# Optimization experiments

Hardware: AMD Instinct MI355X
Metric: run time of the kernel (lower is better)

## Reference

```python
import jax, jax.numpy as jnp
import numpy as np

D, H = 2048, 16
Q_RANK, KV_RANK = 1536, 512
NOPE, ROPE_D, V_D = 128, 64, 128
QK_D = NOPE + ROPE_D  # 192
S, B = 2048, 1
THETA = 10000.0
EPS = 1e-5


def rmsnorm(x, w, eps=EPS):
    return x * jax.lax.rsqrt(jnp.mean(x * x, -1, keepdims=True) + eps) * w


def rope_cos_sin(s, d, theta=THETA):
    inv = 1.0 / (theta ** (jnp.arange(0, d, 2, dtype=jnp.float32) / d))
    f = jnp.arange(s, dtype=jnp.float32)[:, None] * inv[None, :]  # [s, d//2]
    emb = jnp.concatenate([f, f], -1)  # [s, d]
    return jnp.cos(emb), jnp.sin(emb)


def apply_rope(x, cos, sin):
    # DeepSeek-V3 variant: de-interleave consecutive pairs into [even | odd] halves first
    b, h, s, d = x.shape
    x = x.reshape(b, h, s, d // 2, 2).transpose(0, 1, 2, 4, 3).reshape(b, h, s, d)
    x1, x2 = jnp.split(x, 2, -1)
    rot = jnp.concatenate([-x2, x1], -1)
    return x * cos + rot * sin


def setup_inputs() -> dict:
    key = jax.random.key(0)
    ks = jax.random.split(key, 10)
    s = 0.02
    return {
        "x": jax.random.normal(ks[0], (S, B, D), jnp.float32),
        "norm1_w": jnp.ones((D,), jnp.float32),
        "q_a_w": jax.random.normal(ks[1], (D, Q_RANK), jnp.float32) * s,
        "q_a_ln_w": jnp.ones((Q_RANK,), jnp.float32),
        "q_b_w": jax.random.normal(ks[2], (Q_RANK, H * QK_D), jnp.float32) * s,
        "kv_a_w": jax.random.normal(ks[3], (D, KV_RANK + ROPE_D), jnp.float32) * s,
        "kv_a_ln_w": jnp.ones((KV_RANK,), jnp.float32),
        "kv_b_w": jax.random.normal(ks[4], (KV_RANK, H * (NOPE + V_D)), jnp.float32) * s,
        "o_w": jax.random.normal(ks[5], (H * V_D, D), jnp.float32) * s,
        "norm2_w": jnp.ones((D,), jnp.float32),
        "ffn_w1": jax.random.normal(ks[6], (D, 4 * D), jnp.float32) * s,
        "ffn_b1": jnp.zeros((4 * D,), jnp.float32),
        "ffn_w2": jax.random.normal(ks[7], (4 * D, D), jnp.float32) * s,
        "ffn_b2": jnp.zeros((D,), jnp.float32),
    }


def reference(x, norm1_w, q_a_w, q_a_ln_w, q_b_w, kv_a_w, kv_a_ln_w, kv_b_w, o_w,
              norm2_w, ffn_w1, ffn_b1, ffn_w2, ffn_b2):
    # x: [S, B, D] (block transposes to [B, S, D] before MLA)
    hs = jnp.swapaxes(rmsnorm(x, norm1_w), 0, 1)  # [B, S, D]
    b, s, _ = hs.shape

    # --- MLA: low-rank Q and KV with decoupled RoPE ---
    q = rmsnorm(hs @ q_a_w, q_a_ln_w) @ q_b_w                    # [B, S, H*192]
    q = q.reshape(b, s, H, QK_D).transpose(0, 2, 1, 3)           # [B, H, S, 192]
    q_nope, q_pe = q[..., :NOPE], q[..., NOPE:]

    kv_a = hs @ kv_a_w                                           # [B, S, 576]
    c_kv, k_pe = kv_a[..., :KV_RANK], kv_a[..., KV_RANK:]        # [B,S,512], [B,S,64]
    kv = rmsnorm(c_kv, kv_a_ln_w) @ kv_b_w                       # [B, S, H*256]
    kv = kv.reshape(b, s, H, NOPE + V_D).transpose(0, 2, 1, 3)   # [B, H, S, 256]
    k_nope, v = kv[..., :NOPE], kv[..., NOPE:]

    cos, sin = rope_cos_sin(s, ROPE_D)
    q_pe = apply_rope(q_pe, cos, sin)                            # [B, H, S, 64]
    k_pe = apply_rope(k_pe[:, None, :, :], cos, sin)             # [B, 1, S, 64]

    q_full = jnp.concatenate([q_nope, q_pe], -1)                 # [B, H, S, 192]
    k_full = jnp.concatenate([k_nope, jnp.broadcast_to(k_pe, (b, H, s, ROPE_D))], -1)

    scores = jnp.einsum('bhqd,bhkd->bhqk', q_full, k_full) * (1.0 / np.sqrt(QK_D))
    causal = jnp.tril(jnp.ones((s, s), bool))
    scores = jnp.where(causal, scores, jnp.finfo(scores.dtype).min)
    attn = jax.nn.softmax(scores, -1)
    out = jnp.einsum('bhqk,bhkd->bhqd', attn, v)                 # [B, H, S, 128]
    out = out.transpose(0, 2, 1, 3).reshape(b, s, H * V_D) @ o_w # [B, S, D]

    x = x + jnp.swapaxes(out, 0, 1)                              # residual, back to [S,B,D]

    # --- FFN (exact GELU) ---
    h2 = rmsnorm(x, norm2_w)
    ffn = jax.nn.gelu(h2 @ ffn_w1 + ffn_b1, approximate=False) @ ffn_w2 + ffn_b2
    return x + ffn
```

## Files before the change

kernel.cpp:

```cpp
#include <hip/hip_runtime.h>
#include <hip/hip_bf16.h>

typedef __hip_bfloat16 bf16;
using bf16x8 = __attribute__((ext_vector_type(8))) __bf16;
using f32x4  = __attribute__((ext_vector_type(4))) float;

#define S_   2048
#define D_   2048
#define H_   16
#define QR_  1536
#define KVR_ 512
#define NOPE_ 128
#define ROPE_ 64
#define VD_  128
#define QKD_ 192
#define EPS_ 1e-5f
#define QKVN 2112

#define GLDS16(g, l) \
    __builtin_amdgcn_global_load_lds((const __attribute__((address_space(1))) void*)(g), \
                                     (__attribute__((address_space(3))) void*)(l), 16, 0, 0)

#define PIPE_WAIT4 asm volatile("s_waitcnt vmcnt(4)\n\ts_barrier" ::: "memory")
#define PIPE_WAIT0 asm volatile("s_waitcnt vmcnt(0)\n\ts_barrier" ::: "memory")

__global__ __launch_bounds__(256) void gemm_k(
    const bf16* __restrict__ A, const bf16* __restrict__ BT, void* __restrict__ Cv,
    const float* __restrict__ bias, const float* __restrict__ res,
    int M, int N, int K, int lda, int ldb, int ldc,
    long long strideA, long long strideB, long long strideC,
    int mode, int causal, int ksplit, int kchunk)
{
    int bn = blockIdx.x, bm = blockIdx.y;
    int bzC = blockIdx.z;
    int bz = bzC, kc = 0;
    if (ksplit > 1) { kc = bzC % ksplit; bz = bzC / ksplit; }
    if (causal == 1 && bn > bm) return;
    A  += (size_t)bz * strideA;
    BT += (size_t)bz * strideB;

    int k_end = K;
    if (causal == 2) { int kl = (bm + 1) * 128; if (kl < k_end) k_end = kl; }
    int k_begin = kc * kchunk;
    if (k_begin + kchunk < k_end) k_end = k_begin + kchunk;
    if (k_begin >= k_end) return;
    int nIter = (k_end - k_begin) >> 5;

    __shared__ bf16 sA[3 * 128 * 32];
    __shared__ bf16 sB[3 * 128 * 32];

    int tid  = threadIdx.x;
    int lane = tid & 63, wave = tid >> 6;
    int wr = wave >> 1, wc = wave & 1;
    int fr = lane & 15, fq = lane >> 4;

    int row0 = bm * 128, col0 = bn * 128;

    int srow = wave * 16 + (lane >> 2);
    int sko  = (lane & 3) * 8;
    const bf16* ga0 = A + (size_t)(row0 + srow) * lda + sko;
    const bf16* ga1 = ga0 + (size_t)64 * lda;
    int bn0 = col0 + srow;      if (bn0 > N - 1) bn0 = N - 1;
    int bn1 = col0 + srow + 64; if (bn1 > N - 1) bn1 = N - 1;
    const bf16* gb0 = BT + (size_t)bn0 * ldb + sko;
    const bf16* gb1 = BT + (size_t)bn1 * ldb + sko;
    bf16* lA0 = &sA[(wave * 16) * 32];
    bf16* lA1 = &sA[(64 + wave * 16) * 32];
    bf16* lB0 = &sB[(wave * 16) * 32];
    bf16* lB1 = &sB[(64 + wave * 16) * 32];

#define STAGE(ofs, k0) do {                  \
        GLDS16(ga0 + (k0), lA0 + (ofs));     \
        GLDS16(ga1 + (k0), lA1 + (ofs));     \
        GLDS16(gb0 + (k0), lB0 + (ofs));     \
        GLDS16(gb1 + (k0), lB1 + (ofs));     \
    } while (0)

    f32x4 acc[4][4] = {};

#define COMPUTE(ofs) do {                                                           \
        bf16x8 af[4], bv[4];                                                        \
        _Pragma("unroll")                                                           \
        for (int i = 0; i < 4; ++i)                                                 \
            af[i] = *(const bf16x8*)&sA[(ofs) + (wr*64 + i*16 + fr)*32 + fq*8];     \
        _Pragma("unroll")                                                           \
        for (int j = 0; j < 4; ++j)                                                 \
            bv[j] = *(const bf16x8*)&sB[(ofs) + (wc*64 + j*16 + fr)*32 + fq*8];     \
        _Pragma("unroll")                                                           \
        for (int i = 0; i < 4; ++i)                                                 \
            _Pragma("unroll")                                                       \
            for (int j = 0; j < 4; ++j)                                             \
                acc[i][j] = __builtin_amdgcn_mfma_f32_16x16x32_bf16(af[i], bv[j], acc[i][j], 0, 0, 0); \
    } while (0)

    STAGE(0, k_begin);
    if (nIter > 1) STAGE(4096, k_begin + 32);

    int curo = 0, pfo = 8192;
    int it = 0;
    for (; it < nIter - 1; ++it) {
        PIPE_WAIT4;
        if (it + 2 < nIter) STAGE(pfo, k_begin + (it + 2) * 32);
        COMPUTE(curo);
        curo += 4096; if (curo == 12288) curo = 0;
        pfo  += 4096; if (pfo  == 12288) pfo  = 0;
    }
    PIPE_WAIT0;
    COMPUTE(curo);
#undef STAGE
#undef COMPUTE

    #pragma unroll
    for (int i = 0; i < 4; ++i) {
        #pragma unroll
        for (int j = 0; j < 4; ++j) {
            int gc = col0 + wc*64 + j*16 + fr;
            if (gc >= N) continue;
            #pragma unroll
            for (int r = 0; r < 4; ++r) {
                int gr = row0 + wr*64 + i*16 + fq*4 + r;
                float v = acc[i][j][r];
                size_t off = (size_t)bzC * strideC + (size_t)gr * ldc + gc;
                if (mode == 0 || mode == 6) {
                    ((float*)Cv)[off] = v;
                } else if (mode == 1) {
                    ((bf16*)Cv)[off] = __float2bfloat16(v);
                } else if (mode == 2) {
                    ((float*)Cv)[off] = v + res[(size_t)gr * ldc + gc];
                } else if (mode == 3) {
                    float t = v + bias[gc];
                    t = 0.5f * t * (1.0f + erff(t * 0.70710678118654752f));
                    ((bf16*)Cv)[off] = __float2bfloat16(t);
                } else {
                    ((float*)Cv)[off] = v + bias[gc] + res[(size_t)gr * ldc + gc];
                }
            }
        }
    }
}

__global__ __launch_bounds__(512, 2) void gemm256_k(
    const bf16* __restrict__ A, const bf16* __restrict__ BT, void* __restrict__ Cv,
    const float* __restrict__ bias,
    int M, int N, int K, int lda, int ldb, int ldc,
    long long strideC, int mode, int kchunk)
{
    int bn = blockIdx.x, bm = blockIdx.y, kc = blockIdx.z;
    int k_begin = kc * kchunk;
    int k_end = (k_begin + kchunk < K) ? (k_begin + kchunk) : K;
    int NT = (k_end - k_begin) >> 6;

    __shared__ __align__(16) bf16 sA[2 * 256 * 64];
    __shared__ __align__(16) bf16 sB[2 * 256 * 64];

    int tid = threadIdx.x;
    int lane = tid & 63, w = tid >> 6;
    int wr = w >> 2, wc = w & 3;
    int fr = lane & 15, fq = lane >> 4;
    int row0 = bm * 256, col0 = bn * 256;

    int g0 = tid, g1 = tid + 512;
    int r0 = g0 >> 3, l0 = (g0 & 7) ^ (r0 & 7);
    int r1 = g1 >> 3, l1 = (g1 & 7) ^ (r1 & 7);
    const bf16* gA00 = A + (size_t)(row0 + r0) * lda + k_begin + l0 * 8;
    const bf16* gA01 = A + (size_t)(row0 + r1) * lda + k_begin + l1 * 8;
    const bf16* gA10 = gA00 + (size_t)128 * lda;
    const bf16* gA11 = gA01 + (size_t)128 * lda;
    int c00 = col0 + r0;       if (c00 > N - 1) c00 = N - 1;
    int c01 = col0 + r1;       if (c01 > N - 1) c01 = N - 1;
    int c10 = col0 + 128 + r0; if (c10 > N - 1) c10 = N - 1;
    int c11 = col0 + 128 + r1; if (c11 > N - 1) c11 = N - 1;
    const bf16* gB00 = BT + (size_t)c00 * ldb + k_begin + l0 * 8;
    const bf16* gB01 = BT + (size_t)c01 * ldb + k_begin + l1 * 8;
    const bf16* gB10 = BT + (size_t)c10 * ldb + k_begin + l0 * 8;
    const bf16* gB11 = BT + (size_t)c11 * ldb + k_begin + l1 * 8;

#define ST_HALF(arr, bofs, p0, p1, t) do {                                  \
        GLDS16((p0) + (size_t)(t) * 64, (arr) + (bofs) + w * 512);          \
        GLDS16((p1) + (size_t)(t) * 64, (arr) + (bofs) + w * 512 + 4096);   \
    } while (0)
#define ST_A0(b, t) ST_HALF(sA, (b) * 16384,        gA00, gA01, t)
#define ST_A1(b, t) ST_HALF(sA, (b) * 16384 + 8192, gA10, gA11, t)
#define ST_B0(b, t) ST_HALF(sB, (b) * 16384,        gB00, gB01, t)
#define ST_B1(b, t) ST_HALF(sB, (b) * 16384 + 8192, gB10, gB11, t)

    int arow = (wr * 128 + fr) * 64;
    int brow = (wc * 64 + fr) * 64;
    int pk0 = (fq ^ (fr & 7)) * 8;
    int pk1 = pk0 ^ 32;

    f32x4 acc[8][4] = {};

#define MFMA_Q(AF, BF, IOFF, JOFF) do {                                     \
        __builtin_amdgcn_s_setprio(1);                                      \
        _Pragma("unroll")                                                   \
        for (int m = 0; m < 4; ++m)                                         \
            _Pragma("unroll")                                               \
            for (int n = 0; n < 2; ++n)                                     \
                acc[(IOFF)+m][(JOFF)+n] = __builtin_amdgcn_mfma_f32_16x16x32_bf16( \
                    AF[m][0], BF[n][0], acc[(IOFF)+m][(JOFF)+n], 0, 0, 0);  \
        _Pragma("unroll")                                                   \
        for (int m = 0; m < 4; ++m)                                         \
            _Pragma("unroll")                                               \
            for (int n = 0; n < 2; ++n)                                     \
                acc[(IOFF)+m][(JOFF)+n] = __builtin_amdgcn_mfma_f32_16x16x32_bf16( \
                    AF[m][1], BF[n][1], acc[(IOFF)+m][(JOFF)+n], 0, 0, 0);  \
        __builtin_amdgcn_s_setprio(0);                                      \
    } while (0)

    ST_A0(0, 0); ST_A1(0, 0); ST_B0(0, 0); ST_B1(0, 0);
    if (NT > 1) { ST_B0(1, 1); ST_B1(1, 1); ST_A0(1, 1); }
    if (NT > 1) asm volatile("s_waitcnt vmcnt(6)" ::: "memory");
    else        asm volatile("s_waitcnt vmcnt(0)" ::: "memory");
    __builtin_amdgcn_s_barrier();

    for (int t = 0; t < NT; ++t) {
        int buf = t & 1;
        int sbase = buf * 16384;
        bf16x8 af[4][2], blo[2][2], bhi[2][2];

        #pragma unroll
        for (int m = 0; m < 4; ++m) {
            af[m][0] = *(const bf16x8*)&sA[sbase + arow + m*1024 + pk0];
            af[m][1] = *(const bf16x8*)&sA[sbase + arow + m*1024 + pk1];
        }
        #pragma unroll
        for (int n = 0; n < 2; ++n) {
            blo[n][0] = *(const bf16x8*)&sB[sbase + brow + n*1024 + pk0];
            blo[n][1] = *(const bf16x8*)&sB[sbase + brow + n*1024 + pk1];
        }
        if (t + 1 < NT) ST_A1((t + 1) & 1, t + 1);
        asm volatile("s_waitcnt lgkmcnt(8)" ::: "memory");
        __builtin_amdgcn_s_barrier();
        asm volatile("s_waitcnt lgkmcnt(0)" ::: "memory");
        __builtin_amdgcn_sched_barrier(0);
        MFMA_Q(af, blo, 0, 0);
        __builtin_amdgcn_s_barrier();

        #pragma unroll
        for (int n = 0; n < 2; ++n) {
            bhi[n][0] = *(const bf16x8*)&sB[sbase + brow + (n+2)*1024 + pk0];
            bhi[n][1] = *(const bf16x8*)&sB[sbase + brow + (n+2)*1024 + pk1];
        }
        if (t + 2 < NT) ST_B0(buf, t + 2);
        __builtin_amdgcn_s_barrier();
        asm volatile("s_waitcnt lgkmcnt(0)" ::: "memory");
        __builtin_amdgcn_sched_barrier(0);
        MFMA_Q(af, bhi, 0, 2);
        __builtin_amdgcn_s_barrier();

        #pragma unroll
        for (int m = 0; m < 4; ++m) {
            af[m][0] = *(const bf16x8*)&sA[sbase + arow + 4096 + m*1024 + pk0];
            af[m][1] = *(const bf16x8*)&sA[sbase + arow + 4096 + m*1024 + pk1];
        }
        if (t + 2 < NT) ST_B1(buf, t + 2);
        __builtin_amdgcn_s_barrier();
        asm volatile("s_waitcnt lgkmcnt(0)" ::: "memory");
        __builtin_amdgcn_sched_barrier(0);
        MFMA_Q(af, blo, 4, 0);
        __builtin_amdgcn_s_barrier();

        if (t + 2 < NT) ST_A0(buf, t + 2);
        if (t < NT - 2) asm volatile("s_waitcnt vmcnt(6)" ::: "memory");
        else            asm volatile("s_waitcnt vmcnt(0)" ::: "memory");
        __builtin_amdgcn_s_barrier();
        MFMA_Q(af, bhi, 4, 2);
        __builtin_amdgcn_s_barrier();
    }
#undef MFMA_Q
#undef ST_A0
#undef ST_A1
#undef ST_B0
#undef ST_B1
#undef ST_HALF

    #pragma unroll
    for (int i = 0; i < 8; ++i) {
        #pragma unroll
        for (int j = 0; j < 4; ++j) {
            int gc = col0 + wc*64 + j*16 + fr;
            if (gc >= N) continue;
            #pragma unroll
            for (int r = 0; r < 4; ++r) {
                int gr = row0 + wr*128 + i*16 + fq*4 + r;
                float v = acc[i][j][r];
                size_t off = (size_t)kc * strideC + (size_t)gr * ldc + gc;
                if (mode == 0 || mode == 6) {
                    ((float*)Cv)[off] = v;
                } else if (mode == 1) {
                    ((bf16*)Cv)[off] = __float2bfloat16(v);
                } else {
                    float tt = v + bias[gc];
                    tt = 0.5f * tt * (1.0f + erff(tt * 0.70710678118654752f));
                    ((bf16*)Cv)[off] = __float2bfloat16(tt);
                }
            }
        }
    }
}

__global__ __launch_bounds__(256) void red_k(const float* __restrict__ part,
        long long pstride4, int nch, const float* __restrict__ res,
        const float* __restrict__ bias, long long cols4,
        float* __restrict__ dstF, bf16* __restrict__ dstB, long long n4)
{
    long long i = (long long)blockIdx.x * 256 + threadIdx.x;
    long long stride = (long long)gridDim.x * 256;
    for (; i < n4; i += stride) {
        float4 v = ((const float4*)part)[i];
        for (int k = 1; k < nch; ++k) {
            float4 p = ((const float4*)part)[i + k * pstride4];
            v.x += p.x; v.y += p.y; v.z += p.z; v.w += p.w;
        }
        if (res) {
            float4 rr = ((const float4*)res)[i];
            v.x += rr.x; v.y += rr.y; v.z += rr.z; v.w += rr.w;
        }
        if (bias) {
            float4 b = ((const float4*)bias)[i % cols4];
            v.x += b.x; v.y += b.y; v.z += b.z; v.w += b.w;
        }
        if (dstB) {
            ushort4 o;
            bf16 t0 = __float2bfloat16(v.x); o.x = *(unsigned short*)&t0;
            bf16 t1 = __float2bfloat16(v.y); o.y = *(unsigned short*)&t1;
            bf16 t2 = __float2bfloat16(v.z); o.z = *(unsigned short*)&t2;
            bf16 t3 = __float2bfloat16(v.w); o.w = *(unsigned short*)&t3;
            ((ushort4*)dstB)[i] = o;
        } else {
            ((float4*)dstF)[i] = v;
        }
    }
}

__global__ __launch_bounds__(128) void pv_red(const float* __restrict__ part,
                                              bf16* __restrict__ ao, int grp)
{
    int r = blockIdx.x, head = blockIdx.y, d = threadIdx.x;
    int nv = ((r >> 7) + 4) >> 2;
    const float* p = part + ((size_t)head * 4) * S_ * VD_ + (size_t)r * VD_ + d;
    float s = 0.f;
    for (int k = 0; k < nv; ++k) s += p[(size_t)k * S_ * VD_];
    ao[(size_t)r * (H_ * VD_) + grp * 1024 + head * VD_ + d] = __float2bfloat16(s);
}

__global__ __launch_bounds__(256) void transpose_w(const float* __restrict__ in,
                                                   bf16* __restrict__ out, int R, int C)
{
    __shared__ float t[32][33];
    int c0 = blockIdx.x * 32, r0 = blockIdx.y * 32;
    int tx = threadIdx.x, ty = threadIdx.y;
    for (int j = ty; j < 32; j += 8) {
        int r = r0 + j, c = c0 + tx;
        t[j][tx] = (r < R && c < C) ? in[(size_t)r * C + c] : 0.f;
    }
    __syncthreads();
    for (int j = ty; j < 32; j += 8) {
        int c = c0 + j, r = r0 + tx;
        if (c < C && r < R) out[(size_t)c * R + r] = __float2bfloat16(t[tx][j]);
    }
}

__global__ __launch_bounds__(256) void transpose_v(const bf16* __restrict__ kv,
                                                   bf16* __restrict__ vT)
{
    __shared__ bf16 t[32][33];
    int h = blockIdx.z;
    int d0 = blockIdx.x * 32, s0 = blockIdx.y * 32;
    int tx = threadIdx.x, ty = threadIdx.y;
    for (int j = ty; j < 32; j += 8)
        t[j][tx] = kv[(size_t)(s0 + j) * (H_*256) + h*256 + 128 + d0 + tx];
    __syncthreads();
    for (int j = ty; j < 32; j += 8)
        vT[((size_t)h * VD_ + d0 + j) * S_ + s0 + tx] = t[tx][j];
}

__global__ __launch_bounds__(256) void rmsnorm_k(const float* __restrict__ in,
                                                 const float* __restrict__ w,
                                                 bf16* __restrict__ out,
                                                 int cols, int istride, int ostride)
{
    int row = blockIdx.x, tid = threadIdx.x;
    const float* ip = in + (size_t)row * istride;
    bf16* op = out + (size_t)row * ostride;
    float ss = 0.f;
    for (int c = tid; c < cols; c += 256) { float v = ip[c]; ss = fmaf(v, v, ss); }
    for (int o = 32; o > 0; o >>= 1) ss += __shfl_down(ss, o, 64);
    __shared__ float red[4];
    __shared__ float s_sc;
    int wave = tid >> 6, lane = tid & 63;
    if (lane == 0) red[wave] = ss;
    __syncthreads();
    if (tid == 0) s_sc = rsqrtf((red[0]+red[1]+red[2]+red[3]) / (float)cols + EPS_);
    __syncthreads();
    float sc = s_sc;
    for (int c = tid; c < cols; c += 256)
        op[c] = __float2bfloat16(ip[c] * sc * w[c]);
}

#define ROPE_LC 0.28782313662425575f

__global__ __launch_bounds__(192) void build_q(const bf16* __restrict__ q,
                                               bf16* __restrict__ qf)
{
    int s = blockIdx.x, h = blockIdx.y, t = threadIdx.x;
    const float scale = 0.07216878364870323f;
    const bf16* src = q + (size_t)s * (H_*QKD_) + h * QKD_;
    bf16* dst = qf + ((size_t)h * S_ + s) * QKD_;
    if (t < NOPE_) {
        dst[t] = __float2bfloat16(__bfloat162float(src[t]) * scale);
    } else {
        int i = (t - NOPE_) & 31;
        bool hi = (t - NOPE_) >= 32;
        float a = __bfloat162float(src[NOPE_ + 2*i]);
        float b = __bfloat162float(src[NOPE_ + 2*i + 1]);
        float inv = __expf(-(float)i * ROPE_LC);
        float f = (float)s * inv, c, sn;
        sincosf(f, &sn, &c);
        float v = hi ? (b * c + a * sn) : (a * c - b * sn);
        dst[t] = __float2bfloat16(v * scale);
    }
}

__global__ __launch_bounds__(192) void build_k(const bf16* __restrict__ kv,
                                               const float* __restrict__ qakva32,
                                               bf16* __restrict__ kf)
{
    int s = blockIdx.x, h = blockIdx.y, t = threadIdx.x;
    const bf16* src = kv + (size_t)s * (H_*256) + h * 256;
    bf16* dst = kf + ((size_t)h * S_ + s) * QKD_;
    if (t < NOPE_) {
        dst[t] = src[t];
    } else {
        int i = (t - NOPE_) & 31;
        bool hi = (t - NOPE_) >= 32;
        const float* pe = qakva32 + (size_t)s * QKVN + (QR_ + KVR_);
        float a = pe[2*i], b = pe[2*i + 1];
        float inv = __expf(-(float)i * ROPE_LC);
        float f = (float)s * inv, c, sn;
        sincosf(f, &sn, &c);
        dst[t] = __float2bfloat16(hi ? (b * c + a * sn) : (a * c - b * sn));
    }
}

__global__ __launch_bounds__(256) void softmax_k(bf16* __restrict__ Sc)
{
    int q = blockIdx.x, h = blockIdx.y;
    bf16* row = Sc + ((size_t)h * S_ + q) * S_;
    int n = q + 1;
    int klim = ((q >> 7) + 1) << 7;
    int tid = threadIdx.x, lane = tid & 63, wave = tid >> 6;
    __shared__ float red[4];
    __shared__ float bc;

    float v[8];
    #pragma unroll
    for (int k = 0; k < 8; ++k) {
        int c = tid + k * 256;
        v[k] = (c < n) ? __bfloat162float(row[c]) : -3.0e38f;
    }
    float mx = v[0];
    #pragma unroll
    for (int k = 1; k < 8; ++k) mx = fmaxf(mx, v[k]);
    for (int o = 32; o > 0; o >>= 1) mx = fmaxf(mx, __shfl_down(mx, o, 64));
    if (lane == 0) red[wave] = mx;
    __syncthreads();
    if (tid == 0) bc = fmaxf(fmaxf(red[0], red[1]), fmaxf(red[2], red[3]));
    __syncthreads();
    float m = bc;
    float sum = 0.f;
    #pragma unroll
    for (int k = 0; k < 8; ++k) {
        int c = tid + k * 256;
        v[k] = (c < n) ? __expf(v[k] - m) : 0.f;
        sum += v[k];
    }
    for (int o = 32; o > 0; o >>= 1) sum += __shfl_down(sum, o, 64);
    __syncthreads();
    if (lane == 0) red[wave] = sum;
    __syncthreads();
    if (tid == 0) bc = 1.0f / (red[0] + red[1] + red[2] + red[3]);
    __syncthreads();
    float inv = bc;
    #pragma unroll
    for (int k = 0; k < 8; ++k) {
        int c = tid + k * 256;
        if (c < klim) row[c] = __float2bfloat16(c < n ? v[k] * inv : 0.f);
    }
}

static inline void gemm(hipStream_t st, const bf16* A, const bf16* BT, void* C,
                        const float* bias, const float* res,
                        int M, int N, int K, int lda, int ldb, int ldc,
                        long long sA, long long sB, long long sC,
                        int batch, int mode, int causal, int ksplit = 1, int kchunk = 0)
{
    if (kchunk == 0) kchunk = K;
    dim3 g((N + 127) / 128, M / 128, batch * ksplit);
    gemm_k<<<g, 256, 0, st>>>(A, BT, C, bias, res, M, N, K, lda, ldb, ldc,
                              sA, sB, sC, mode, causal, ksplit, kchunk);
}

static inline void gemm256(hipStream_t st, const bf16* A, const bf16* BT, void* C,
                           const float* bias, int M, int N, int K,
                           int lda, int ldb, int ldc, long long sC,
                           int mode, int ksplit = 1, int kchunk = 0)
{
    if (kchunk == 0) kchunk = K;
    dim3 g((N + 255) / 256, M / 256, ksplit);
    gemm256_k<<<g, 512, 0, st>>>(A, BT, C, bias, M, N, K, lda, ldb, ldc,
                                 sC, mode, kchunk);
}

static inline void transw(hipStream_t st, const float* in, bf16* out, int R, int C)
{
    dim3 g((C + 31) / 32, (R + 31) / 32);
    transpose_w<<<g, dim3(32, 8), 0, st>>>(in, out, R, C);
}

extern "C" void kernel_launch(void* const* d_in, const int* in_sizes, int n_in,
                              void* d_out, int out_size, void* d_ws, size_t ws_size,
                              hipStream_t stream)
{
    const float* x        = (const float*)d_in[0];
    const float* norm1_w  = (const float*)d_in[1];
    const float* q_a_w    = (const float*)d_in[2];
    const float* q_a_ln_w = (const float*)d_in[3];
    const float* q_b_w    = (const float*)d_in[4];
    const float* kv_a_w   = (const float*)d_in[5];
    const float* kv_a_ln_w= (const float*)d_in[6];
    const float* kv_b_w   = (const float*)d_in[7];
    const float* o_w      = (const float*)d_in[8];
    const float* norm2_w  = (const float*)d_in[9];
    const float* ffn_w1   = (const float*)d_in[10];
    const float* ffn_b1   = (const float*)d_in[11];
    const float* ffn_w2   = (const float*)d_in[12];
    const float* ffn_b2   = (const float*)d_in[13];
    float* out = (float*)d_out;

    size_t off = 0;
    auto alloc = [&](size_t bytes) -> void* {
        void* p = (char*)d_ws + off;
        off += (bytes + 255) & ~(size_t)255;
        return p;
    };
    bf16*  hs     = (bf16*) alloc((size_t)S_*D_*2);
    bf16*  wqakvT = (bf16*) alloc((size_t)QKVN*D_*2);
    bf16*  wqbT   = (bf16*) alloc((size_t)(H_*QKD_)*QR_*2);
    bf16*  wkvbT  = (bf16*) alloc((size_t)(H_*(NOPE_+VD_))*KVR_*2);
    bf16*  woT    = (bf16*) alloc((size_t)D_*(H_*VD_)*2);
    bf16*  wf1T   = (bf16*) alloc((size_t)(4*D_)*D_*2);
    bf16*  wf2T   = (bf16*) alloc((size_t)D_*(4*D_)*2);
    float* qakva32= (float*)alloc((size_t)S_*QKVN*4);
    bf16*  qln    = (bf16*) alloc((size_t)S_*QR_*2);
    bf16*  kvln   = (bf16*) alloc((size_t)S_*KVR_*2);
    bf16*  qb     = (bf16*) alloc((size_t)S_*H_*QKD_*2);
    bf16*  kvb    = (bf16*) alloc((size_t)S_*H_*(NOPE_+VD_)*2);
    bf16*  qf     = (bf16*) alloc((size_t)H_*S_*QKD_*2);
    bf16*  kf     = (bf16*) alloc((size_t)H_*S_*QKD_*2);
    bf16*  vT     = (bf16*) alloc((size_t)H_*VD_*S_*2);
    bf16*  Sc     = (bf16*) alloc((size_t)8*S_*S_*2);
    float* qakvaP = (float*)Sc;
    float* qbP    = (float*)Sc;
    float* pvP    = (float*)qakva32;
    float* oP     = (float*)Sc;
    float* f2P    = (float*)d_ws;
    float* x2     = qakva32;
    bf16*  h2     = qb;
    bf16*  ao     = kvb;
    bf16*  a1     = Sc;

    transw(stream, q_a_w,  wqakvT,                    D_,  QR_);
    transw(stream, kv_a_w, wqakvT + (size_t)QR_ * D_, D_,  KVR_+ROPE_);
    transw(stream, q_b_w,  wqbT,  QR_, H_*QKD_);
    transw(stream, kv_b_w, wkvbT, KVR_, H_*(NOPE_+VD_));
    transw(stream, o_w,    woT,   H_*VD_, D_);
    transw(stream, ffn_w1, wf1T,  D_,  4*D_);
    transw(stream, ffn_w2, wf2T,  4*D_, D_);

    rmsnorm_k<<<S_, 256, 0, stream>>>(x, norm1_w, hs, D_, D_, D_);

    gemm256(stream, hs, wqakvT, qakvaP, nullptr, S_, QKVN, D_, D_, D_, QKVN,
            (long long)S_*QKVN, 6, 3, 768);
    red_k<<<1024, 256, 0, stream>>>(qakvaP, (long long)S_*QKVN/4, 3, nullptr, nullptr, 1,
                                    qakva32, nullptr, (long long)S_*QKVN/4);

    rmsnorm_k<<<S_, 256, 0, stream>>>(qakva32, q_a_ln_w, qln, QR_, QKVN, QR_);
    gemm256(stream, qln, wqbT, qbP, nullptr, S_, H_*QKD_, QR_, QR_, QR_, H_*QKD_,
            (long long)S_*(H_*QKD_), 6, 2, 768);
    red_k<<<1024, 256, 0, stream>>>(qbP, (long long)S_*(H_*QKD_)/4, 2, nullptr, nullptr, 1,
                                    nullptr, qb, (long long)S_*(H_*QKD_)/4);

    rmsnorm_k<<<S_, 256, 0, stream>>>(qakva32 + QR_, kv_a_ln_w, kvln, KVR_, QKVN, KVR_);
    gemm(stream, kvln, wkvbT, kvb, nullptr, nullptr, S_, H_*(NOPE_+VD_), KVR_,
         KVR_, KVR_, H_*(NOPE_+VD_), 0, 0, 0, 1, 1, 0);

    build_q<<<dim3(S_, H_), 192, 0, stream>>>(qb, qf);
    build_k<<<dim3(S_, H_), 192, 0, stream>>>(kvb, qakva32, kf);
    transpose_v<<<dim3(VD_/32, S_/32, H_), dim3(32, 8), 0, stream>>>(kvb, vT);

    for (int g = 0; g < 2; ++g) {
        const bf16* qfg = qf + (size_t)g * 8 * S_ * QKD_;
        const bf16* kfg = kf + (size_t)g * 8 * S_ * QKD_;
        const bf16* vTg = vT + (size_t)g * 8 * VD_ * S_;
        gemm(stream, qfg, kfg, Sc, nullptr, nullptr,
             S_, S_, QKD_, QKD_, QKD_, S_,
             (long long)S_*QKD_, (long long)S_*QKD_, (long long)S_*S_, 8, 1, 1);
        softmax_k<<<dim3(S_, 8), 256, 0, stream>>>(Sc);
        gemm(stream, Sc, vTg, pvP, nullptr, nullptr,
             S_, VD_, S_, S_, S_, VD_,
             (long long)S_*S_, (long long)VD_*S_, (long long)S_*VD_, 8, 6, 2, 4, 512);
        pv_red<<<dim3(S_, 8), 128, 0, stream>>>(pvP, ao, g);
    }

    gemm256(stream, ao, woT, oP, nullptr, S_, D_, H_*VD_, H_*VD_, H_*VD_, D_,
            (long long)S_*D_, 6, 4, 512);
    red_k<<<1024, 256, 0, stream>>>(oP, (long long)S_*D_/4, 4, x, nullptr, 1,
                                    x2, nullptr, (long long)S_*D_/4);

    rmsnorm_k<<<S_, 256, 0, stream>>>(x2, norm2_w, h2, D_, D_, D_);
    gemm256(stream, h2, wf1T, a1, ffn_b1, S_, 4*D_, D_, D_, D_, 4*D_,
            0, 3, 1, 0);
    gemm256(stream, a1, wf2T, f2P, nullptr, S_, D_, 4*D_, 4*D_, 4*D_, D_,
            (long long)S_*D_, 6, 4, 2048);
    red_k<<<1024, 256, 0, stream>>>(f2P, (long long)S_*D_/4, 4, x2, ffn_b2, D_/4,
                                    out, nullptr, (long long)S_*D_/4);
}
```

Measured before the change: 962.7 us.

## Prefetch next tile's LDS fragments into registers during final MFMA quadrant

Restructures the GEMM main loop so the A/B low fragments for the next k-tile are read from LDS while the last MFMA quadrant of the current tile runs, with separate register sets for the low and high halves. Each quadrant's LDS reads now overlap the preceding MFMA block instead of stalling on lgkmcnt(0) before it. The cost is higher VGPR pressure from keeping four fragment sets live, which could lower occupancy or cause spills, and the reordered waits and barriers must still respect the buffer reuse hazards.

```diff
diff --git a/kernel.cpp b/kernel.cpp
--- a/kernel.cpp
+++ b/kernel.cpp
@@ -214,58 +214,75 @@
     else        asm volatile("s_waitcnt vmcnt(0)" ::: "memory");
     __builtin_amdgcn_s_barrier();
 
+    bf16x8 a_lo[4][2], a_hi[4][2], b_lo[2][2], b_hi[2][2];
+    #pragma unroll
+    for (int m = 0; m < 4; ++m) {
+        a_lo[m][0] = *(const bf16x8*)&sA[arow + m*1024 + pk0];
+        a_lo[m][1] = *(const bf16x8*)&sA[arow + m*1024 + pk1];
+    }
+    #pragma unroll
+    for (int n = 0; n < 2; ++n) {
+        b_lo[n][0] = *(const bf16x8*)&sB[brow + n*1024 + pk0];
+        b_lo[n][1] = *(const bf16x8*)&sB[brow + n*1024 + pk1];
+    }
+
     for (int t = 0; t < NT; ++t) {
         int buf = t & 1;
         int sbase = buf * 16384;
-        bf16x8 af[4][2], blo[2][2], bhi[2][2];
+        int nbase = sbase ^ 16384;
+
+        #pragma unroll
+        for (int n = 0; n < 2; ++n) {
+            b_hi[n][0] = *(const bf16x8*)&sB[sbase + brow + (n+2)*1024 + pk0];
+            b_hi[n][1] = *(const bf16x8*)&sB[sbase + brow + (n+2)*1024 + pk1];
+        }
+        if (t + 1 < NT) ST_A1((t + 1) & 1, t + 1);
+        __builtin_amdgcn_sched_barrier(0);
+        __builtin_amdgcn_s_barrier();
+        asm volatile("s_waitcnt lgkmcnt(4)" ::: "memory");
+        __builtin_amdgcn_sched_barrier(0);
+        MFMA_Q(a_lo, b_lo, 0, 0);
+        __builtin_amdgcn_s_barrier();
 
         #pragma unroll
         for (int m = 0; m < 4; ++m) {
-            af[m][0] = *(const bf16x8*)&sA[sbase + arow + m*1024 + pk0];
-            af[m][1] = *(const bf16x8*)&sA[sbase + arow + m*1024 + pk1];
-        }
-        #pragma unroll
-        for (int n = 0; n < 2; ++n) {
-            blo[n][0] = *(const bf16x8*)&sB[sbase + brow + n*1024 + pk0];
-            blo[n][1] = *(const bf16x8*)&sB[sbase + brow + n*1024 + pk1];
-        }
-        if (t + 1 < NT) ST_A1((t + 1) & 1, t + 1);
+            a_hi[m][0] = *(const bf16x8*)&sA[sbase + arow + 4096 + m*1024 + pk0];
+            a_hi[m][1] = *(const bf16x8*)&sA[sbase + arow + 4096 + m*1024 + pk1];
+        }
+        if (t + 2 < NT) ST_B0(buf, t + 2);
+        __builtin_amdgcn_sched_barrier(0);
+        __builtin_amdgcn_s_barrier();
         asm volatile("s_waitcnt lgkmcnt(8)" ::: "memory");
+        __builtin_amdgcn_sched_barrier(0);
+        MFMA_Q(a_lo, b_hi, 0, 2);
+        __builtin_amdgcn_s_barrier();
+
+        if (t + 2 < NT) ST_B1(buf, t + 2);
+        __builtin_amdgcn_sched_barrier(0);
         __builtin_amdgcn_s_barrier();
         asm volatile("s_waitcnt lgkmcnt(0)" ::: "memory");
         __builtin_amdgcn_sched_barrier(0);
-        MFMA_Q(af, blo, 0, 0);
-        __builtin_amdgcn_s_barrier();
-
-        #pragma unroll
-        for (int n = 0; n < 2; ++n) {
-            bhi[n][0] = *(const bf16x8*)&sB[sbase + brow + (n+2)*1024 + pk0];
-            bhi[n][1] = *(const bf16x8*)&sB[sbase + brow + (n+2)*1024 + pk1];
-        }
-        if (t + 2 < NT) ST_B0(buf, t + 2);
-        __builtin_amdgcn_s_barrier();
-        asm volatile("s_waitcnt lgkmcnt(0)" ::: "memory");
-        __builtin_amdgcn_sched_barrier(0);
-        MFMA_Q(af, bhi, 0, 2);
-        __builtin_amdgcn_s_barrier();
-
-        #pragma unroll
-        for (int m = 0; m < 4; ++m) {
-            af[m][0] = *(const bf16x8*)&sA[sbase + arow + 4096 + m*1024 + pk0];
-            af[m][1] = *(const bf16x8*)&sA[sbase + arow + 4096 + m*1024 + pk1];
-        }
-        if (t + 2 < NT) ST_B1(buf, t + 2);
-        __builtin_amdgcn_s_barrier();
-        asm volatile("s_waitcnt lgkmcnt(0)" ::: "memory");
-        __builtin_amdgcn_sched_barrier(0);
-        MFMA_Q(af, blo, 4, 0);
+        MFMA_Q(a_hi, b_lo, 4, 0);
         __builtin_amdgcn_s_barrier();
 
         if (t + 2 < NT) ST_A0(buf, t + 2);
         if (t < NT - 2) asm volatile("s_waitcnt vmcnt(6)" ::: "memory");
         else            asm volatile("s_waitcnt vmcnt(0)" ::: "memory");
         __builtin_amdgcn_s_barrier();
-        MFMA_Q(af, bhi, 4, 2);
+        if (t + 1 < NT) {
+            #pragma unroll
+            for (int m = 0; m < 4; ++m) {
+                a_lo[m][0] = *(const bf16x8*)&sA[nbase + arow + m*1024 + pk0];
+                a_lo[m][1] = *(const bf16x8*)&sA[nbase + arow + m*1024 + pk1];
+            }
+            #pragma unroll
+            for (int n = 0; n < 2; ++n) {
+                b_lo[n][0] = *(const bf16x8*)&sB[nbase + brow + n*1024 + pk0];
+                b_lo[n][1] = *(const bf16x8*)&sB[nbase + brow + n*1024 + pk1];
+            }
+        }
+        __builtin_amdgcn_sched_barrier(0);
+        MFMA_Q(a_hi, b_hi, 4, 2);
         __builtin_amdgcn_s_barrier();
     }
 #undef MFMA_Q
```

Result: slower. 1.151 ms (+19.6%).
